# Performance work log

Measured on AMD Instinct MI355X. Metric: run time of the kernel, lower is better.

Reference implementation:

```python
import jax, jax.numpy as jnp
import numpy as np

HIDDEN = 2048
N_HEADS = 16
HEAD_DIM = HIDDEN // N_HEADS
MAX_POS = 4096
ROPE_THETA = 10000.0
B, S = 2, 4096


def rotate_half(x):
    d = x.shape[-1] // 2
    return jnp.concatenate([-x[..., d:], x[..., :d]], axis=-1)


def make_rope_cache(seq_len, dim, base):
    inv_freq = 1.0 / (base ** (np.arange(0, dim, 2, dtype=np.float32) / dim))
    t = np.arange(seq_len, dtype=np.float32)
    freqs = np.einsum('i,j->ij', t, inv_freq)
    emb = np.concatenate([freqs, freqs], axis=-1)
    return jnp.asarray(np.cos(emb)), jnp.asarray(np.sin(emb))


def setup_inputs() -> dict:
    key = jax.random.key(0)
    k1, k2, k3, k4, k5, k6 = jax.random.split(key, 6)
    hidden_states = jax.random.normal(k1, (B, S, HIDDEN), dtype=jnp.float32)
    # causal additive mask [B,1,S,S]
    causal = jnp.where(jnp.tril(jnp.ones((S, S), dtype=bool)), 0.0, -1e9).astype(jnp.float32)
    attention_mask = jnp.broadcast_to(causal[None, None], (B, 1, S, S))
    position_ids = jnp.broadcast_to(jnp.arange(S, dtype=jnp.int64)[None], (B, S))
    scale = 0.02
    Wq = jax.random.normal(k2, (HIDDEN, HIDDEN), dtype=jnp.float32) * scale
    Wk = jax.random.normal(k3, (HIDDEN, HIDDEN), dtype=jnp.float32) * scale
    Wv = jax.random.normal(k4, (HIDDEN, HIDDEN), dtype=jnp.float32) * scale
    Wo = jax.random.normal(k5, (HIDDEN, HIDDEN), dtype=jnp.float32) * scale
    return {"hidden_states": hidden_states, "attention_mask": attention_mask,
            "position_ids": position_ids, "Wq": Wq, "Wk": Wk, "Wv": Wv, "Wo": Wo}


def reference(hidden_states, attention_mask, position_ids, Wq, Wk, Wv, Wo):
    bsz, q_len, _ = hidden_states.shape
    # projections (torch Linear: x @ W.T; here W stored as [in,out] -> x @ W)
    q = (hidden_states @ Wq).reshape(bsz, q_len, N_HEADS, HEAD_DIM).transpose(0, 2, 1, 3)
    k = (hidden_states @ Wk).reshape(bsz, q_len, N_HEADS, HEAD_DIM).transpose(0, 2, 1, 3)
    v = (hidden_states @ Wv).reshape(bsz, q_len, N_HEADS, HEAD_DIM).transpose(0, 2, 1, 3)
    cos_c, sin_c = make_rope_cache(q_len, HEAD_DIM, ROPE_THETA)
    cos = cos_c[position_ids][:, None]  # [B,1,S,Dh]
    sin = sin_c[position_ids][:, None]
    q = q * cos + rotate_half(q) * sin
    k = k * cos + rotate_half(k) * sin
    scores = jnp.einsum('bhqd,bhkd->bhqk', q, k) / jnp.sqrt(jnp.float32(HEAD_DIM))
    scores = scores + attention_mask
    probs = jax.nn.softmax(scores.astype(jnp.float32), axis=-1).astype(q.dtype)
    attn = jnp.einsum('bhqk,bhkd->bhqd', probs, v)
    attn = attn.transpose(0, 2, 1, 3).reshape(bsz, q_len, HIDDEN)
    return attn @ Wo
```

## Files before the change

### kernel.cpp

```cpp
#include <hip/hip_runtime.h>

#define HID 2048
#define NHEADS 16
#define DHEAD 128
#define BB 2
#define SS 4096
#define MTOT (BB * SS)

typedef __attribute__((ext_vector_type(8))) short short8;
typedef __attribute__((ext_vector_type(8))) unsigned short ushort8;
typedef __attribute__((ext_vector_type(4))) float floatx4;
typedef __attribute__((ext_vector_type(16))) float floatx16;

static __device__ __forceinline__ ushort f2bf(float f) {
  unsigned x = __float_as_uint(f);
  return (ushort)((x + 0x7fffu + ((x >> 16) & 1u)) >> 16);
}
static __device__ __forceinline__ float bf2f(ushort u) {
  return __uint_as_float(((unsigned)u) << 16);
}
static __device__ __forceinline__ unsigned cvtpk_bf16(float lo, float hi) {
  unsigned r;
  asm("v_cvt_pk_bf16_f32 %0, %1, %2" : "=v"(r) : "v"(lo), "v"(hi));
  return r;
}
static __device__ __forceinline__ void pl32swap(unsigned& a, unsigned& b) {
  asm volatile("v_permlane32_swap_b32 %0, %1" : "+v"(a), "+v"(b));
}
static __device__ __forceinline__ floatx16 fz16() {
  floatx16 z;
#pragma unroll
  for (int i = 0; i < 16; i++) z[i] = 0.f;
  return z;
}

#define GL16(g, l)                                                   \
  __builtin_amdgcn_global_load_lds(                                  \
      (const __attribute__((address_space(1))) unsigned int*)(g),    \
      (__attribute__((address_space(3))) unsigned int*)(l), 16, 0, 0)

__global__ __launch_bounds__(256) void k_prep(const float* __restrict__ X,
                                              ushort* __restrict__ Xb,
                                              const float* __restrict__ Wq,
                                              const float* __restrict__ Wk,
                                              const float* __restrict__ Wv,
                                              const float* __restrict__ Wo,
                                              ushort* __restrict__ Wqt,
                                              ushort* __restrict__ Wkt,
                                              ushort* __restrict__ Wvt,
                                              ushort* __restrict__ Wot,
                                              float* __restrict__ cosT,
                                              float* __restrict__ sinT) {
  __shared__ float tile[64][65];
  int id = blockIdx.x, t = threadIdx.x;
  if (id < 2048) {
    int i = id * 256 + t;
    const int n4 = MTOT * HID / 4, stride = 2048 * 256;
    for (; i < n4; i += stride) {
      float4 v = reinterpret_cast<const float4*>(X)[i];
      ushort4 u;
      u.x = f2bf(v.x); u.y = f2bf(v.y); u.z = f2bf(v.z); u.w = f2bf(v.w);
      reinterpret_cast<ushort4*>(Xb)[i] = u;
    }
  } else if (id < 6144) {
    int w = (id - 2048) >> 10;
    int bid = (id - 2048) & 1023;
    const float* W = (w == 0) ? Wq : (w == 1) ? Wk : (w == 2) ? Wv : Wo;
    ushort* Wt = (w == 0) ? Wqt : (w == 1) ? Wkt : (w == 2) ? Wvt : Wot;
    int n0 = (bid & 31) * 64, k0 = (bid >> 5) * 64;
#pragma unroll
    for (int i = 0; i < 16; i++) {
      int idx = t + i * 256, r = idx >> 6, c = idx & 63;
      tile[r][c] = W[(size_t)(k0 + r) * HID + n0 + c];
    }
    __syncthreads();
#pragma unroll
    for (int i = 0; i < 16; i++) {
      int idx = t + i * 256, r = idx >> 6, c = idx & 63;
      Wt[(size_t)(n0 + r) * HID + k0 + c] = f2bf(tile[c][r]);
    }
  } else {
    int idx = (id - 6144) * 256 + t;
    int pos = idx >> 6, j = idx & 63;
    float inv = powf(10000.0f, -(float)(2 * j) * (1.0f / 128.0f));
    float a = (float)pos * inv;
    cosT[idx] = cosf(a);
    sinT[idx] = sinf(a);
  }
}

template <int OUT_BF16, int DUAL>
__global__ __launch_bounds__(512, 2) void k_gemm8(const ushort* __restrict__ A,
                                                  const ushort* __restrict__ Bt,
                                                  void* __restrict__ Cp,
                                                  const ushort* __restrict__ Bt2,
                                                  void* __restrict__ Cp2,
                                                  int Mr, int Nc, int Kd) {
  __shared__ ushort As[3][256 * 32];
  __shared__ ushort Bs[3][256 * 32];
  int t = threadIdx.x;
  int lane = t & 63, wid = t >> 6;
  int lrow = lane & 15, lk = lane >> 4;
  int wr = wid >> 2, wc = wid & 3;

  int id = blockIdx.x;
  if (DUAL && id >= 256) {
    Bt = Bt2;
    Cp = Cp2;
    id -= 256;
  }
  int nbx = Nc >> 8;
  int swz = (id & 7) * 32 + (id >> 3);
  int m0 = (swz / nbx) << 8, n0 = (swz % nbx) << 8;

  floatx4 acc[8][4];
#pragma unroll
  for (int i = 0; i < 8; i++)
#pragma unroll
    for (int j = 0; j < 4; j++) acc[i][j] = (floatx4){0.f, 0.f, 0.f, 0.f};

  int arow = t >> 2;
  int acol = (((t & 3) ^ (arow & 3)) << 3);
  const ushort* gA = A + (size_t)(m0 + arow) * Kd + acol;
  const ushort* gB = Bt + (size_t)(n0 + arow) * Kd + acol;

  auto STAGE = [&](int buf, int kt) {
    const ushort* a = gA + kt * 32;
    const ushort* bq = gB + kt * 32;
    GL16(a, (char*)As + buf * 16384 + t * 16);
    GL16(a + (size_t)128 * Kd, (char*)As + buf * 16384 + t * 16 + 8192);
    GL16(bq, (char*)Bs + buf * 16384 + t * 16);
    GL16(bq + (size_t)128 * Kd, (char*)Bs + buf * 16384 + t * 16 + 8192);
  };

  STAGE(0, 0);
  STAGE(1, 1);

  int nk = Kd >> 5;
  for (int tK = 0; tK < nk; ++tK) {
    if (tK + 1 < nk)
      asm volatile("s_waitcnt vmcnt(4)" ::: "memory");
    else
      asm volatile("s_waitcnt vmcnt(0)" ::: "memory");
    __builtin_amdgcn_s_barrier();
    asm volatile("" ::: "memory");
    int buf = tK % 3;
    const char* Ab_ = (const char*)As + buf * 16384;
    const char* Bb_ = (const char*)Bs + buf * 16384;
    short8 af[8], bfr[4];
#pragma unroll
    for (int fm = 0; fm < 8; fm++) {
      int row = wr * 128 + fm * 16 + lrow;
      af[fm] = *reinterpret_cast<const short8*>(
          Ab_ + ((row * 64 + lk * 16) ^ ((row & 3) << 4)));
    }
#pragma unroll
    for (int fn = 0; fn < 4; fn++) {
      int row = wc * 64 + fn * 16 + lrow;
      bfr[fn] = *reinterpret_cast<const short8*>(
          Bb_ + ((row * 64 + lk * 16) ^ ((row & 3) << 4)));
    }
    if (tK + 2 < nk) STAGE((tK + 2) % 3, tK + 2);
    __builtin_amdgcn_s_setprio(1);
#pragma unroll
    for (int fm = 0; fm < 8; fm++)
#pragma unroll
      for (int fn = 0; fn < 4; fn++)
        acc[fm][fn] = __builtin_amdgcn_mfma_f32_16x16x32_bf16(af[fm], bfr[fn],
                                                              acc[fm][fn], 0, 0, 0);
    __builtin_amdgcn_s_setprio(0);
  }

#pragma unroll
  for (int am = 0; am < 8; am++)
#pragma unroll
    for (int an = 0; an < 4; an++)
#pragma unroll
      for (int r = 0; r < 4; r++) {
        int m = m0 + wr * 128 + am * 16 + lk * 4 + r;
        int n = n0 + wc * 64 + an * 16 + lrow;
        if (OUT_BF16)
          ((ushort*)Cp)[(size_t)m * Nc + n] = f2bf(acc[am][an][r]);
        else
          ((float*)Cp)[(size_t)m * Nc + n] = acc[am][an][r];
      }
}

__global__ __launch_bounds__(512, 2) void k_gvrope(const ushort* __restrict__ A,
                                                   const ushort* __restrict__ Bt,
                                                   ushort* __restrict__ Cp,
                                                   ushort* __restrict__ Q,
                                                   ushort* __restrict__ Kb,
                                                   const float* __restrict__ cosT,
                                                   const float* __restrict__ sinT) {
  __shared__ ushort As[3][256 * 32];
  __shared__ ushort Bs[3][256 * 32];
  int t = threadIdx.x;
  if (blockIdx.x >= 256) {
    const float kSc = 0.12751742f;
    int idx = (blockIdx.x - 256) * 512 + t;
    int j8 = (idx & 7) * 8;
    int hh = (idx >> 3) & (NHEADS - 1);
    int srow = idx >> 7;
    int pos = srow & (SS - 1);
    float4 c0 = *reinterpret_cast<const float4*>(&cosT[pos * 64 + j8]);
    float4 c1 = *reinterpret_cast<const float4*>(&cosT[pos * 64 + j8 + 4]);
    float4 s0 = *reinterpret_cast<const float4*>(&sinT[pos * 64 + j8]);
    float4 s1 = *reinterpret_cast<const float4*>(&sinT[pos * 64 + j8 + 4]);
    float cc[8] = {c0.x, c0.y, c0.z, c0.w, c1.x, c1.y, c1.z, c1.w};
    float ss[8] = {s0.x, s0.y, s0.z, s0.w, s1.x, s1.y, s1.z, s1.w};
    size_t base = (size_t)srow * HID + hh * DHEAD + j8;
    ushort8 qa = *reinterpret_cast<ushort8*>(&Q[base]);
    ushort8 qb = *reinterpret_cast<ushort8*>(&Q[base + 64]);
    ushort8 ka = *reinterpret_cast<ushort8*>(&Kb[base]);
    ushort8 kb = *reinterpret_cast<ushort8*>(&Kb[base + 64]);
    ushort8 o1, o2, o3, o4;
#pragma unroll
    for (int i = 0; i < 8; i++) {
      float a1 = bf2f(qa[i]), a2 = bf2f(qb[i]);
      o1[i] = f2bf((a1 * cc[i] - a2 * ss[i]) * kSc);
      o2[i] = f2bf((a2 * cc[i] + a1 * ss[i]) * kSc);
      float b1 = bf2f(ka[i]), b2 = bf2f(kb[i]);
      o3[i] = f2bf(b1 * cc[i] - b2 * ss[i]);
      o4[i] = f2bf(b2 * cc[i] + b1 * ss[i]);
    }
    *reinterpret_cast<ushort8*>(&Q[base]) = o1;
    *reinterpret_cast<ushort8*>(&Q[base + 64]) = o2;
    *reinterpret_cast<ushort8*>(&Kb[base]) = o3;
    *reinterpret_cast<ushort8*>(&Kb[base + 64]) = o4;
    return;
  }

  const int Nc = MTOT, Kd = HID;
  int lane = t & 63, wid = t >> 6;
  int lrow = lane & 15, lk = lane >> 4;
  int wr = wid >> 2, wc = wid & 3;
  int id = blockIdx.x;
  int nbx = Nc >> 8;
  int swz = (id & 7) * 32 + (id >> 3);
  int m0 = (swz / nbx) << 8, n0 = (swz % nbx) << 8;

  floatx4 acc[8][4];
#pragma unroll
  for (int i = 0; i < 8; i++)
#pragma unroll
    for (int j = 0; j < 4; j++) acc[i][j] = (floatx4){0.f, 0.f, 0.f, 0.f};

  int arow = t >> 2;
  int acol = (((t & 3) ^ (arow & 3)) << 3);
  const ushort* gA = A + (size_t)(m0 + arow) * Kd + acol;
  const ushort* gB = Bt + (size_t)(n0 + arow) * Kd + acol;

  auto STAGE = [&](int buf, int kt) {
    const ushort* a = gA + kt * 32;
    const ushort* bq = gB + kt * 32;
    GL16(a, (char*)As + buf * 16384 + t * 16);
    GL16(a + (size_t)128 * Kd, (char*)As + buf * 16384 + t * 16 + 8192);
    GL16(bq, (char*)Bs + buf * 16384 + t * 16);
    GL16(bq + (size_t)128 * Kd, (char*)Bs + buf * 16384 + t * 16 + 8192);
  };

  STAGE(0, 0);
  STAGE(1, 1);

  int nk = Kd >> 5;
  for (int tK = 0; tK < nk; ++tK) {
    if (tK + 1 < nk)
      asm volatile("s_waitcnt vmcnt(4)" ::: "memory");
    else
      asm volatile("s_waitcnt vmcnt(0)" ::: "memory");
    __builtin_amdgcn_s_barrier();
    asm volatile("" ::: "memory");
    int buf = tK % 3;
    const char* Ab_ = (const char*)As + buf * 16384;
    const char* Bb_ = (const char*)Bs + buf * 16384;
    short8 af[8], bfr[4];
#pragma unroll
    for (int fm = 0; fm < 8; fm++) {
      int row = wr * 128 + fm * 16 + lrow;
      af[fm] = *reinterpret_cast<const short8*>(
          Ab_ + ((row * 64 + lk * 16) ^ ((row & 3) << 4)));
    }
#pragma unroll
    for (int fn = 0; fn < 4; fn++) {
      int row = wc * 64 + fn * 16 + lrow;
      bfr[fn] = *reinterpret_cast<const short8*>(
          Bb_ + ((row * 64 + lk * 16) ^ ((row & 3) << 4)));
    }
    if (tK + 2 < nk) STAGE((tK + 2) % 3, tK + 2);
    __builtin_amdgcn_s_setprio(1);
#pragma unroll
    for (int fm = 0; fm < 8; fm++)
#pragma unroll
      for (int fn = 0; fn < 4; fn++)
        acc[fm][fn] = __builtin_amdgcn_mfma_f32_16x16x32_bf16(af[fm], bfr[fn],
                                                              acc[fm][fn], 0, 0, 0);
    __builtin_amdgcn_s_setprio(0);
  }

#pragma unroll
  for (int am = 0; am < 8; am++)
#pragma unroll
    for (int an = 0; an < 4; an++)
#pragma unroll
      for (int r = 0; r < 4; r++) {
        int m = m0 + wr * 128 + am * 16 + lk * 4 + r;
        int n = n0 + wc * 64 + an * 16 + lrow;
        Cp[(size_t)m * Nc + n] = f2bf(acc[am][an][r]);
      }
}

__global__ __launch_bounds__(256, 2) void k_fattn(const ushort* __restrict__ Qg,
                                                  const ushort* __restrict__ Kg,
                                                  const ushort* __restrict__ Vt2,
                                                  ushort* __restrict__ Og) {
  __shared__ ushort Ks[2][32 * 128];
  __shared__ ushort Vs[2][128 * 32];
  int t = threadIdx.x, lane = t & 63, wid = t >> 6;
  int l31 = lane & 31, hi = lane >> 5;
  int id = blockIdx.x;
  int qt = 31 - (id >> 5);
  int h = id & 15, b = (id >> 4) & 1;

  auto STAGE = [&](int buf, int kt) {
    int kv0 = kt * 32;
    const ushort* Kbase = Kg + (size_t)(b * SS + kv0) * HID + h * DHEAD;
    const ushort* Vbase = Vt2 + (size_t)(h * DHEAD) * MTOT + b * SS + kv0;
#pragma unroll
    for (int i = 0; i < 2; i++) {
      int L = t + i * 256;
      int row = L >> 4, cr = L & 15;
      GL16(Kbase + (size_t)row * HID + ((cr ^ (row & 15)) << 3),
           (char*)Ks + buf * 8192 + L * 16);
    }
#pragma unroll
    for (int i = 0; i < 2; i++) {
      int L = t + i * 256;
      int row = L >> 2, cr = L & 3;
      GL16(Vbase + (size_t)row * MTOT + ((cr ^ (row & 3)) << 3),
           (char*)Vs + buf * 8192 + L * 16);
    }
  };

  int q0 = qt * 128;
  int wq0 = q0 + wid * 32;
  int qlane = wq0 + l31;

  short8 qf[8];
  {
    const ushort* qb = Qg + (size_t)(b * SS + qlane) * HID + h * DHEAD + hi * 8;
#pragma unroll
    for (int ks = 0; ks < 8; ks++)
      qf[ks] = *reinterpret_cast<const short8*>(qb + ks * 16);
  }

  floatx16 accO[4];
#pragma unroll
  for (int db = 0; db < 4; db++) accO[db] = fz16();
  float mrow = -1e30f, lsum = 0.f;

  int nkt = (qt + 1) * 4;
  STAGE(0, 0);

  for (int kt = 0; kt < nkt; kt++) {
    int cur = kt & 1;
    int kv0 = kt * 32;
    bool pre = (kt + 1 < nkt);
    if (pre) {
      STAGE(cur ^ 1, kt + 1);
      asm volatile("s_waitcnt vmcnt(4)" ::: "memory");
    } else {
      asm volatile("s_waitcnt vmcnt(0)" ::: "memory");
    }
    __builtin_amdgcn_s_barrier();
    asm volatile("" ::: "memory");

    if (kv0 <= wq0 + 31) {
      const char* Kb_ = (const char*)Ks + cur * 8192;
      floatx16 accS = fz16();
      __builtin_amdgcn_s_setprio(1);
#pragma unroll
      for (int ks = 0; ks < 8; ks++) {
        int row = l31;
        int byte_ = (row * 256 + ks * 32 + hi * 16) ^ ((row & 15) << 4);
        short8 kf = *reinterpret_cast<const short8*>(Kb_ + byte_);
        accS = __builtin_amdgcn_mfma_f32_32x32x16_bf16(kf, qf[ks], accS, 0, 0, 0);
      }
      __builtin_amdgcn_s_setprio(0);

      if (kv0 + 31 > wq0) {
        int kvbase = kv0 + hi * 4;
#pragma unroll
        for (int r = 0; r < 16; r++) {
          int kvi = kvbase + (r & 3) + 8 * (r >> 2);
          if (kvi > qlane) accS[r] = -1e30f;
        }
      }

      float mA = -1e30f, mB = -1e30f, mC = -1e30f, mD = -1e30f;
#pragma unroll
      for (int r = 0; r < 16; r += 4) {
        mA = fmaxf(mA, accS[r]);
        mB = fmaxf(mB, accS[r + 1]);
        mC = fmaxf(mC, accS[r + 2]);
        mD = fmaxf(mD, accS[r + 3]);
      }
      float mx = fmaxf(fmaxf(mA, mB), fmaxf(mC, mD));
      mx = fmaxf(mx, __shfl_xor(mx, 32));
      if (!__all(mx <= mrow + 8.0f)) {
        float mnew = fmaxf(mrow, mx);
        float corr = exp2f(mrow - mnew);
        mrow = mnew;
        lsum *= corr;
#pragma unroll
        for (int db = 0; db < 4; db++)
#pragma unroll
          for (int r = 0; r < 16; r++) accO[db][r] *= corr;
      }

      float sA = 0.f, sB = 0.f, sC = 0.f, sD = 0.f;
#pragma unroll
      for (int r = 0; r < 16; r += 4) {
        float p0 = exp2f(accS[r] - mrow);
        float p1 = exp2f(accS[r + 1] - mrow);
        float p2 = exp2f(accS[r + 2] - mrow);
        float p3 = exp2f(accS[r + 3] - mrow);
        accS[r] = p0; accS[r + 1] = p1; accS[r + 2] = p2; accS[r + 3] = p3;
        sA += p0; sB += p1; sC += p2; sD += p3;
      }
      lsum += ((sA + sB) + (sC + sD));

      const char* Vb_ = (const char*)Vs + cur * 8192;
#pragma unroll
      for (int ks = 0; ks < 2; ks++) {
        int tt = ks;
        unsigned w0 = cvtpk_bf16(accS[8 * tt + 0], accS[8 * tt + 1]);
        unsigned w2 = cvtpk_bf16(accS[8 * tt + 4], accS[8 * tt + 5]);
        pl32swap(w0, w2);
        unsigned w1 = cvtpk_bf16(accS[8 * tt + 2], accS[8 * tt + 3]);
        unsigned w3 = cvtpk_bf16(accS[8 * tt + 6], accS[8 * tt + 7]);
        pl32swap(w1, w3);
        union { unsigned u[4]; short8 v; } pf;
        pf.u[0] = w0; pf.u[1] = w1; pf.u[2] = w2; pf.u[3] = w3;
        __builtin_amdgcn_s_setprio(1);
#pragma unroll
        for (int db = 0; db < 4; db++) {
          int row = db * 32 + l31;
          int byte_ = (row * 64 + ks * 32 + hi * 16) ^ ((row & 3) << 4);
          short8 vf = *reinterpret_cast<const short8*>(Vb_ + byte_);
          accO[db] = __builtin_amdgcn_mfma_f32_32x32x16_bf16(vf, pf.v, accO[db], 0, 0, 0);
        }
        __builtin_amdgcn_s_setprio(0);
      }
    }
    asm volatile("" ::: "memory");
    __builtin_amdgcn_s_barrier();
    asm volatile("" ::: "memory");
  }

  float lt = lsum + __shfl_xor(lsum, 32);
  float inv = 1.0f / lt;
  char* sb = ((wid < 2) ? (char*)Ks : (char*)Vs) + (wid & 1) * 8192;
#pragma unroll
  for (int db = 0; db < 4; db++)
#pragma unroll
    for (int r = 0; r < 16; r += 2) {
      int d = db * 32 + (r & 3) + 8 * (r >> 2) + hi * 4;
      unsigned w = cvtpk_bf16(accO[db][r] * inv, accO[db][r + 1] * inv);
      int byte_ = (l31 * 256 + d * 2) ^ ((l31 & 15) << 4);
      *reinterpret_cast<unsigned*>(sb + byte_) = w;
    }
#pragma unroll
  for (int i = 0; i < 8; i++) {
    int row = i * 4 + (lane >> 4);
    int byte_ = (row * 256 + (lane & 15) * 16) ^ ((row & 15) << 4);
    ushort8 ov = *reinterpret_cast<const ushort8*>(sb + byte_);
    *reinterpret_cast<ushort8*>(Og + (size_t)(b * SS + wq0 + row) * HID + h * DHEAD +
                                (lane & 15) * 8) = ov;
  }
}

extern "C" void kernel_launch(void* const* d_in, const int* in_sizes, int n_in,
                              void* d_out, int out_size, void* d_ws, size_t ws_size,
                              hipStream_t stream) {
  const float* X = (const float*)d_in[0];
  const float* Wq = (const float*)d_in[3];
  const float* Wk = (const float*)d_in[4];
  const float* Wv = (const float*)d_in[5];
  const float* Wo = (const float*)d_in[6];
  float* out = (float*)d_out;

  char* p = (char*)d_ws;
  const size_t szXb = (size_t)MTOT * HID * 2;
  const size_t szW = (size_t)HID * HID * 2;
  ushort* Xb = (ushort*)p;  p += szXb;
  ushort* Wqt = (ushort*)p; p += szW;
  ushort* Wkt = (ushort*)p; p += szW;
  ushort* Wvt = (ushort*)p; p += szW;
  ushort* Wot = (ushort*)p; p += szW;
  ushort* Qb = (ushort*)p;  p += szXb;
  ushort* Kb = (ushort*)p;  p += szXb;
  ushort* Vt2 = (ushort*)p; p += szXb;
  ushort* Ab = (ushort*)p;  p += szXb;
  float* cosT = (float*)p;  p += (size_t)SS * 64 * 4;
  float* sinT = (float*)p;  p += (size_t)SS * 64 * 4;

  k_prep<<<7168, 256, 0, stream>>>(X, Xb, Wq, Wk, Wv, Wo, Wqt, Wkt, Wvt, Wot,
                                   cosT, sinT);

  k_gemm8<1, 1><<<512, 512, 0, stream>>>(Xb, Wqt, Qb, Wkt, Kb, MTOT, HID, HID);
  k_gvrope<<<2304, 512, 0, stream>>>(Wvt, Xb, Vt2, Qb, Kb, cosT, sinT);

  k_fattn<<<1024, 256, 0, stream>>>(Qb, Kb, Vt2, Ab);

  k_gemm8<0, 0><<<256, 512, 0, stream>>>(Ab, Wot, out, nullptr, nullptr, MTOT, HID, HID);
}
```

Before: 528.4 us.

## Enlarge flash attention tiles to 256 queries and 64 KV per step

Retiles the attention kernel to 512-thread blocks covering 256 query rows, with 64-key K/V tiles staged per iteration and two score accumulators per wave. This halves the number of KV iterations and barriers, and amortizes each K/V tile over more query waves. It also replaces exp2f with the raw v_exp_f32 instruction to cut softmax overhead. In exchange, register and LDS pressure rise and there are half as many blocks, which may hurt occupancy and causal load balance.

```diff
diff --git a/kernel.cpp b/kernel.cpp
--- a/kernel.cpp
+++ b/kernel.cpp
@@ -26,6 +26,11 @@
 }
 static __device__ __forceinline__ void pl32swap(unsigned& a, unsigned& b) {
   asm volatile("v_permlane32_swap_b32 %0, %1" : "+v"(a), "+v"(b));
+}
+static __device__ __forceinline__ float exp2_fast(float x) {
+  float r;
+  asm("v_exp_f32 %0, %1" : "=v"(r) : "v"(x));
+  return r;
 }
 static __device__ __forceinline__ floatx16 fz16() {
   floatx16 z;
@@ -310,39 +315,39 @@
       }
 }
 
-__global__ __launch_bounds__(256, 2) void k_fattn(const ushort* __restrict__ Qg,
+__global__ __launch_bounds__(512, 2) void k_fattn(const ushort* __restrict__ Qg,
                                                   const ushort* __restrict__ Kg,
                                                   const ushort* __restrict__ Vt2,
                                                   ushort* __restrict__ Og) {
-  __shared__ ushort Ks[2][32 * 128];
-  __shared__ ushort Vs[2][128 * 32];
+  __shared__ ushort Ks[2][64 * 128];
+  __shared__ ushort Vs[2][128 * 64];
   int t = threadIdx.x, lane = t & 63, wid = t >> 6;
   int l31 = lane & 31, hi = lane >> 5;
   int id = blockIdx.x;
-  int qt = 31 - (id >> 5);
+  int qt = 15 - (id >> 5);
   int h = id & 15, b = (id >> 4) & 1;
 
   auto STAGE = [&](int buf, int kt) {
-    int kv0 = kt * 32;
+    int kv0 = kt * 64;
     const ushort* Kbase = Kg + (size_t)(b * SS + kv0) * HID + h * DHEAD;
     const ushort* Vbase = Vt2 + (size_t)(h * DHEAD) * MTOT + b * SS + kv0;
 #pragma unroll
     for (int i = 0; i < 2; i++) {
-      int L = t + i * 256;
+      int L = t + i * 512;
       int row = L >> 4, cr = L & 15;
       GL16(Kbase + (size_t)row * HID + ((cr ^ (row & 15)) << 3),
-           (char*)Ks + buf * 8192 + L * 16);
+           (char*)Ks + buf * 16384 + L * 16);
     }
 #pragma unroll
     for (int i = 0; i < 2; i++) {
-      int L = t + i * 256;
-      int row = L >> 2, cr = L & 3;
-      GL16(Vbase + (size_t)row * MTOT + ((cr ^ (row & 3)) << 3),
-           (char*)Vs + buf * 8192 + L * 16);
+      int L = t + i * 512;
+      int row = L >> 3, cr = L & 7;
+      GL16(Vbase + (size_t)row * MTOT + ((cr ^ (row & 7)) << 3),
+           (char*)Vs + buf * 16384 + L * 16);
     }
   };
 
-  int q0 = qt * 128;
+  int q0 = qt * 256;
   int wq0 = q0 + wid * 32;
   int qlane = wq0 + l31;
 
@@ -364,7 +369,7 @@
 
   for (int kt = 0; kt < nkt; kt++) {
     int cur = kt & 1;
-    int kv0 = kt * 32;
+    int kv0 = kt * 64;
     bool pre = (kt + 1 < nkt);
     if (pre) {
       STAGE(cur ^ 1, kt + 1);
@@ -376,40 +381,46 @@
     asm volatile("" ::: "memory");
 
     if (kv0 <= wq0 + 31) {
-      const char* Kb_ = (const char*)Ks + cur * 8192;
-      floatx16 accS = fz16();
+      const char* Kb_ = (const char*)Ks + cur * 16384;
+      floatx16 accS[2];
+      accS[0] = fz16(); accS[1] = fz16();
       __builtin_amdgcn_s_setprio(1);
 #pragma unroll
       for (int ks = 0; ks < 8; ks++) {
-        int row = l31;
-        int byte_ = (row * 256 + ks * 32 + hi * 16) ^ ((row & 15) << 4);
-        short8 kf = *reinterpret_cast<const short8*>(Kb_ + byte_);
-        accS = __builtin_amdgcn_mfma_f32_32x32x16_bf16(kf, qf[ks], accS, 0, 0, 0);
+#pragma unroll
+        for (int kvb = 0; kvb < 2; kvb++) {
+          int row = kvb * 32 + l31;
+          int byte_ = (row * 256 + ks * 32 + hi * 16) ^ ((row & 15) << 4);
+          short8 kf = *reinterpret_cast<const short8*>(Kb_ + byte_);
+          accS[kvb] = __builtin_amdgcn_mfma_f32_32x32x16_bf16(kf, qf[ks], accS[kvb], 0, 0, 0);
+        }
       }
       __builtin_amdgcn_s_setprio(0);
 
-      if (kv0 + 31 > wq0) {
+      if (kv0 + 63 > wq0) {
         int kvbase = kv0 + hi * 4;
 #pragma unroll
-        for (int r = 0; r < 16; r++) {
-          int kvi = kvbase + (r & 3) + 8 * (r >> 2);
-          if (kvi > qlane) accS[r] = -1e30f;
-        }
+        for (int kvb = 0; kvb < 2; kvb++)
+#pragma unroll
+          for (int r = 0; r < 16; r++) {
+            int kvi = kvbase + kvb * 32 + (r & 3) + 8 * (r >> 2);
+            if (kvi > qlane) accS[kvb][r] = -1e30f;
+          }
       }
 
       float mA = -1e30f, mB = -1e30f, mC = -1e30f, mD = -1e30f;
 #pragma unroll
       for (int r = 0; r < 16; r += 4) {
-        mA = fmaxf(mA, accS[r]);
-        mB = fmaxf(mB, accS[r + 1]);
-        mC = fmaxf(mC, accS[r + 2]);
-        mD = fmaxf(mD, accS[r + 3]);
+        mA = fmaxf(mA, fmaxf(accS[0][r], accS[1][r]));
+        mB = fmaxf(mB, fmaxf(accS[0][r + 1], accS[1][r + 1]));
+        mC = fmaxf(mC, fmaxf(accS[0][r + 2], accS[1][r + 2]));
+        mD = fmaxf(mD, fmaxf(accS[0][r + 3], accS[1][r + 3]));
       }
       float mx = fmaxf(fmaxf(mA, mB), fmaxf(mC, mD));
       mx = fmaxf(mx, __shfl_xor(mx, 32));
       if (!__all(mx <= mrow + 8.0f)) {
         float mnew = fmaxf(mrow, mx);
-        float corr = exp2f(mrow - mnew);
+        float corr = exp2_fast(mrow - mnew);
         mrow = mnew;
         lsum *= corr;
 #pragma unroll
@@ -420,25 +431,28 @@
 
       float sA = 0.f, sB = 0.f, sC = 0.f, sD = 0.f;
 #pragma unroll
-      for (int r = 0; r < 16; r += 4) {
-        float p0 = exp2f(accS[r] - mrow);
-        float p1 = exp2f(accS[r + 1] - mrow);
-        float p2 = exp2f(accS[r + 2] - mrow);
-        float p3 = exp2f(accS[r + 3] - mrow);
-        accS[r] = p0; accS[r + 1] = p1; accS[r + 2] = p2; accS[r + 3] = p3;
-        sA += p0; sB += p1; sC += p2; sD += p3;
-      }
+      for (int kvb = 0; kvb < 2; kvb++)
+#pragma unroll
+        for (int r = 0; r < 16; r += 4) {
+          float p0 = exp2_fast(accS[kvb][r] - mrow);
+          float p1 = exp2_fast(accS[kvb][r + 1] - mrow);
+          float p2 = exp2_fast(accS[kvb][r + 2] - mrow);
+          float p3 = exp2_fast(accS[kvb][r + 3] - mrow);
+          accS[kvb][r] = p0; accS[kvb][r + 1] = p1;
+          accS[kvb][r + 2] = p2; accS[kvb][r + 3] = p3;
+          sA += p0; sB += p1; sC += p2; sD += p3;
+        }
       lsum += ((sA + sB) + (sC + sD));
 
-      const char* Vb_ = (const char*)Vs + cur * 8192;
-#pragma unroll
-      for (int ks = 0; ks < 2; ks++) {
-        int tt = ks;
-        unsigned w0 = cvtpk_bf16(accS[8 * tt + 0], accS[8 * tt + 1]);
-        unsigned w2 = cvtpk_bf16(accS[8 * tt + 4], accS[8 * tt + 5]);
+      const char* Vb_ = (const char*)Vs + cur * 16384;
+#pragma unroll
+      for (int ks = 0; ks < 4; ks++) {
+        int kvb = ks >> 1, tt = ks & 1;
+        unsigned w0 = cvtpk_bf16(accS[kvb][8 * tt + 0], accS[kvb][8 * tt + 1]);
+        unsigned w2 = cvtpk_bf16(accS[kvb][8 * tt + 4], accS[kvb][8 * tt + 5]);
         pl32swap(w0, w2);
-        unsigned w1 = cvtpk_bf16(accS[8 * tt + 2], accS[8 * tt + 3]);
-        unsigned w3 = cvtpk_bf16(accS[8 * tt + 6], accS[8 * tt + 7]);
+        unsigned w1 = cvtpk_bf16(accS[kvb][8 * tt + 2], accS[kvb][8 * tt + 3]);
+        unsigned w3 = cvtpk_bf16(accS[kvb][8 * tt + 6], accS[kvb][8 * tt + 7]);
         pl32swap(w1, w3);
         union { unsigned u[4]; short8 v; } pf;
         pf.u[0] = w0; pf.u[1] = w1; pf.u[2] = w2; pf.u[3] = w3;
@@ -446,7 +460,7 @@
 #pragma unroll
         for (int db = 0; db < 4; db++) {
           int row = db * 32 + l31;
-          int byte_ = (row * 64 + ks * 32 + hi * 16) ^ ((row & 3) << 4);
+          int byte_ = (row * 128 + ks * 32 + hi * 16) ^ ((row & 7) << 4);
           short8 vf = *reinterpret_cast<const short8*>(Vb_ + byte_);
           accO[db] = __builtin_amdgcn_mfma_f32_32x32x16_bf16(vf, pf.v, accO[db], 0, 0, 0);
         }
@@ -460,7 +474,7 @@
 
   float lt = lsum + __shfl_xor(lsum, 32);
   float inv = 1.0f / lt;
-  char* sb = ((wid < 2) ? (char*)Ks : (char*)Vs) + (wid & 1) * 8192;
+  char* sb = ((wid < 4) ? (char*)Ks : (char*)Vs) + (wid & 3) * 8192;
 #pragma unroll
   for (int db = 0; db < 4; db++)
 #pragma unroll
@@ -511,7 +525,7 @@
   k_gemm8<1, 1><<<512, 512, 0, stream>>>(Xb, Wqt, Qb, Wkt, Kb, MTOT, HID, HID);
   k_gvrope<<<2304, 512, 0, stream>>>(Wvt, Xb, Vt2, Qb, Kb, cosT, sinT);
 
-  k_fattn<<<1024, 256, 0, stream>>>(Qb, Kb, Vt2, Ab);
+  k_fattn<<<512, 512, 0, stream>>>(Qb, Kb, Vt2, Ab);
 
   k_gemm8<0, 0><<<256, 512, 0, stream>>>(Ab, Wot, out, nullptr, nullptr, MTOT, HID, HID);
 }
```

Measured after the change: 486.7 us, median of 2. -7.9%, faster.
